# Kernel tuning notes

Hardware: AMD Instinct MI355X
Metric: run time of the kernel (lower is better)

The kernel has to match this reference:

```python
import jax, jax.numpy as jnp
import numpy as np
import math

B, S, E = 2, 2048, 2048
H = 16
DH = E // H            # 128
L = 64                 # latent_dim
EB = 128               # effective block size (== block_size, adjuster init = log(block_size))
KB = 4 * EB            # kv block size = 512


def setup_inputs() -> dict:
    key = jax.random.key(0)
    ks = jax.random.split(key, 16)
    s_e = 1.0 / math.sqrt(E)
    s_dh = 1.0 / math.sqrt(DH)
    return {
        "x": jax.random.normal(ks[0], (B, S, E), jnp.float32),
        "Wq": jax.random.normal(ks[1], (E, E), jnp.float32) * s_e,
        "bq": jnp.zeros((E,), jnp.float32),
        "Wk": jax.random.normal(ks[2], (E, E), jnp.float32) * s_e,
        "bk": jnp.zeros((E,), jnp.float32),
        "Wv": jax.random.normal(ks[3], (E, E), jnp.float32) * s_e,
        "bv": jnp.zeros((E,), jnp.float32),
        "Wo": jax.random.normal(ks[4], (E, E), jnp.float32) * s_e,
        "bo": jnp.zeros((E,), jnp.float32),
        "Wql": jax.random.normal(ks[5], (DH, L), jnp.float32) * s_dh,
        "bql": jnp.zeros((L,), jnp.float32),
        "Wkl": jax.random.normal(ks[6], (DH, L), jnp.float32) * s_dh,
        "bkl": jnp.zeros((L,), jnp.float32),
        "Wm": jax.random.normal(ks[7], (DH, DH), jnp.float32) * s_dh,
        "bm": jnp.zeros((DH,), jnp.float32),
    }


def _split_heads(t):
    # [B,S,E] -> [B,H,S,DH]
    return t.reshape(B, S, H, DH).transpose(0, 2, 1, 3)


def reference(x, Wq, bq, Wk, bk, Wv, bv, Wo, bo, Wql, bql, Wkl, bkl, Wm, bm):
    q = _split_heads(x @ Wq + bq)
    k = _split_heads(x @ Wk + bk)
    v = _split_heads(x @ Wv + bv)

    # elu+1 feature maps on latent projections
    q_lat = jax.nn.elu(q @ Wql + bql) + 1.0  # [B,H,S,L]
    k_lat = jax.nn.elu(k @ Wkl + bkl) + 1.0  # [B,H,S,L]

    nq, nk = S // EB, S // KB
    qb = q_lat.reshape(B, H, nq, EB, L)
    kb = k_lat.reshape(B, H, nk, KB, L)
    vb = v.reshape(B, H, nk, KB, DH)

    scale = 1.0 / math.sqrt(L)
    # per-(q block, kv block) scores: [B,H,nq,nk,EB,KB]
    scores = jnp.einsum("bhqel,bhkfl->bhqkef", qb, kb) * scale
    # softmax independently over each kv block (axis = f), then SUM over kv blocks
    probs = jax.nn.softmax(scores, axis=-1)
    out = jnp.einsum("bhqkef,bhkfd->bhqed", probs, vb)  # [B,H,nq,EB,DH]
    out = out.reshape(B, H, S, DH)

    # latent mixer: Linear(head_dim) -> gelu
    mixed = jax.nn.gelu(out @ Wm + bm)

    y = mixed.transpose(0, 2, 1, 3).reshape(B, S, E)
    return y @ Wo + bo
```

## Files before the change

### kernel.cpp

```cpp
#include <hip/hip_runtime.h>
#include <stdint.h>
#include <math.h>

#define B_ 2
#define S_ 2048
#define E_ 2048
#define H_ 16
#define DH_ 128
#define L_ 64

typedef unsigned short u16;
typedef __attribute__((ext_vector_type(4))) float f32x4;
typedef __attribute__((ext_vector_type(8))) short short8;
typedef __attribute__((ext_vector_type(4))) short short4v;

__device__ __forceinline__ u16 f2bf(float f) {
    union { float f; uint32_t u; } c; c.f = f;
    uint32_t u = c.u + 0x7fff + ((c.u >> 16) & 1);
    return (u16)(u >> 16);
}
__device__ __forceinline__ u16 f2bf_ru(float f) {
    union { float f; uint32_t u; } c; c.f = f;
    return (u16)((c.u + 0x8000u) >> 16);
}
__device__ __forceinline__ float bf2f(u16 h) {
    union { uint32_t u; float f; } c; c.u = ((uint32_t)h) << 16;
    return c.f;
}
__device__ __forceinline__ float elu1(float x) {
    return x > 0.f ? x + 1.f : __expf(x);
}
__device__ __forceinline__ float gelu_tanh(float x) {
    float z = 0.7978845608028654f * (x + 0.044715f * x * x * x);
    float az = fabsf(z);
    float e = __expf(-2.f * az);
    float t = (1.f - e) / (1.f + e);
    t = (z >= 0.f) ? t : -t;
    return 0.5f * x * (1.f + t);
}
__device__ __forceinline__ void async16(u16* lds_dst, const u16* g_src) {
    __builtin_amdgcn_global_load_lds(
        (const __attribute__((address_space(1))) uint32_t*)g_src,
        (__attribute__((address_space(3))) uint32_t*)lds_dst, 16, 0, 0);
}
__device__ __forceinline__ int swz_off(int row, int chunk) {
    return ((chunk ^ (row & 7)) << 3);
}

__global__ __launch_bounds__(256) void cvt_bf16(const float* __restrict__ in,
                                                u16* __restrict__ out, int n8) {
    for (int i = blockIdx.x * 256 + threadIdx.x; i < n8; i += gridDim.x * 256) {
        float4 a = reinterpret_cast<const float4*>(in)[2 * i];
        float4 b = reinterpret_cast<const float4*>(in)[2 * i + 1];
        u16 u[8] __attribute__((aligned(16)));
        u[0] = f2bf(a.x); u[1] = f2bf(a.y); u[2] = f2bf(a.z); u[3] = f2bf(a.w);
        u[4] = f2bf(b.x); u[5] = f2bf(b.y); u[6] = f2bf(b.z); u[7] = f2bf(b.w);
        reinterpret_cast<int4*>(out)[i] = *(const int4*)u;
    }
}

__device__ void wtrans_body(u16* sp, const float* __restrict__ W,
                            u16* __restrict__ Wt, int K, int N, int bx, int by) {
    const int tid = threadIdx.x;
    const int n0 = bx * 64, k0 = by * 64;
    const int c4 = (tid & 15) * 4, r = tid >> 4;
    #pragma unroll
    for (int i = 0; i < 4; i++) {
        int row = r + 16 * i;
        float4 v = *reinterpret_cast<const float4*>(&W[(size_t)(k0 + row) * N + n0 + c4]);
        sp[(c4 + 0) * 68 + row] = f2bf(v.x); sp[(c4 + 1) * 68 + row] = f2bf(v.y);
        sp[(c4 + 2) * 68 + row] = f2bf(v.z); sp[(c4 + 3) * 68 + row] = f2bf(v.w);
    }
    __syncthreads();
    #pragma unroll
    for (int i = 0; i < 4; i++) {
        int nr = r + 16 * i;
        ushort4 o = *reinterpret_cast<const ushort4*>(&sp[nr * 68 + c4]);
        *reinterpret_cast<ushort4*>(&Wt[(size_t)(n0 + nr) * K + k0 + c4]) = o;
    }
}

__global__ __launch_bounds__(256) void wtrans(const float* __restrict__ W,
                                              u16* __restrict__ Wt, int K, int N) {
    __shared__ u16 sp[64 * 68];
    wtrans_body(sp, W, Wt, K, N, blockIdx.x, blockIdx.y);
}

__global__ __launch_bounds__(256) void small_prep(
    const float* __restrict__ Wm, const float* __restrict__ Wql,
    const float* __restrict__ Wkl, const float* __restrict__ bq,
    const float* __restrict__ bk, const float* __restrict__ bv,
    const float* __restrict__ bql, const float* __restrict__ bkl,
    u16* __restrict__ Wmt, u16* __restrict__ Wqlt, u16* __restrict__ Wklt,
    float* __restrict__ beff)
{
    __shared__ u16 sp[64 * 68];
    const int blk = blockIdx.x, tid = threadIdx.x;
    if (blk < 4) {
        wtrans_body(sp, Wm, Wmt, 128, 128, blk & 1, blk >> 1);
    } else if (blk < 6) {
        wtrans_body(sp, Wql, Wqlt, 128, 64, 0, blk - 4);
    } else if (blk < 8) {
        wtrans_body(sp, Wkl, Wklt, 128, 64, 0, blk - 6);
    } else if (blk < 16) {
        const float* b  = (blk < 12) ? bq : bk;
        const float* Wl = (blk < 12) ? Wql : Wkl;
        const float* bl = (blk < 12) ? bql : bkl;
        int outoff = (blk < 12) ? 0 : 1024;
        int t = ((blk - 8) & 3) * 256 + tid;
        int h = t >> 6, n = t & 63;
        float s = bl[n];
        for (int d = 0; d < 128; d++) s += b[h * 128 + d] * Wl[d * 64 + n];
        beff[outoff + t] = s;
    } else {
        int t = (blk - 16) * 256 + tid;
        int h = t >> 7, n = t & 127;
        float s = 0.f;
        for (int d = 0; d < 128; d++) s += bv[h * 128 + d] * Wm[d * 128 + n];
        beff[2048 + t] = s;
    }
}

__device__ void weff_body(u16* lds, const float* __restrict__ W,
                          const u16* __restrict__ Wlt, u16* __restrict__ Wefft,
                          int outoff, int kblk, int h)
{
    const int tid = threadIdx.x, l = tid & 63, w = tid >> 6;
    const int k0 = kblk * 128;

    #pragma unroll
    for (int i = 0; i < 4; i++) {
        int lin = i * 256 + tid, row = lin >> 4, c = lin & 15;
        async16(&lds[lin * 8], &Wlt[row * 128 + swz_off(row, c)]);
    }
    #pragma unroll
    for (int i = 0; i < 16; i++) {
        int e = (i * 256 + tid) * 4;
        int row = e >> 7, ec = e & 127;
        float4 v4 = *reinterpret_cast<const float4*>(
            &W[(size_t)(k0 + row) * E_ + h * DH_ + ec]);
        u16 u[4] __attribute__((aligned(8)));
        u[0] = f2bf(v4.x); u[1] = f2bf(v4.y); u[2] = f2bf(v4.z); u[3] = f2bf(v4.w);
        int chunk = ec >> 3, half = (ec >> 2) & 1;
        *reinterpret_cast<uint64_t*>(
            &lds[8192 + row * 128 + swz_off(row, chunk) + half * 4]) = *(const uint64_t*)u;
    }
    __syncthreads();

    f32x4 zero = {0.f, 0.f, 0.f, 0.f};
    f32x4 acc[8];
    #pragma unroll
    for (int nt = 0; nt < 8; nt++) acc[nt] = zero;
    #pragma unroll
    for (int ks = 0; ks < 4; ks++) {
        int arow = 16 * w + (l & 15);
        short8 af = *reinterpret_cast<const short8*>(
            &lds[arow * 128 + swz_off(arow, ks * 4 + (l >> 4))]);
        #pragma unroll
        for (int nt = 0; nt < 8; nt++) {
            int brow = 16 * nt + (l & 15);
            short8 bf = *reinterpret_cast<const short8*>(
                &lds[8192 + brow * 128 + swz_off(brow, ks * 4 + (l >> 4))]);
            acc[nt] = __builtin_amdgcn_mfma_f32_16x16x32_bf16(af, bf, acc[nt], 0, 0, 0);
        }
    }
    #pragma unroll
    for (int nt = 0; nt < 8; nt++) {
        int kc = k0 + 16 * nt + (l & 15);
        #pragma unroll
        for (int j = 0; j < 4; j++) {
            int nl = 16 * w + (l >> 4) * 4 + j;
            Wefft[(size_t)(outoff + h * 64 + nl) * E_ + kc] = f2bf(acc[nt][j]);
        }
    }
}

__device__ void weffv_body(u16* lds, const float* __restrict__ Wv,
                           const u16* __restrict__ Wmt, u16* __restrict__ Wv2t,
                           int eblk, int h)
{
    const int tid = threadIdx.x, l = tid & 63, w = tid >> 6;
    const int e0 = eblk * 128;

    #pragma unroll
    for (int i = 0; i < 8; i++) {
        int lin = i * 256 + tid, row = lin >> 4, c = lin & 15;
        async16(&lds[lin * 8], &Wmt[row * 128 + swz_off(row, c)]);
    }
    #pragma unroll
    for (int i = 0; i < 16; i++) {
        int e = (i * 256 + tid) * 4;
        int row = e >> 7, ec = e & 127;
        float4 v4 = *reinterpret_cast<const float4*>(
            &Wv[(size_t)(e0 + row) * E_ + h * DH_ + ec]);
        u16 u[4] __attribute__((aligned(8)));
        u[0] = f2bf(v4.x); u[1] = f2bf(v4.y); u[2] = f2bf(v4.z); u[3] = f2bf(v4.w);
        int chunk = ec >> 3, half = (ec >> 2) & 1;
        *reinterpret_cast<uint64_t*>(
            &lds[16384 + row * 128 + swz_off(row, chunk) + half * 4]) = *(const uint64_t*)u;
    }
    __syncthreads();

    f32x4 zero = {0.f, 0.f, 0.f, 0.f};
    f32x4 acc[2][8];
    #pragma unroll
    for (int mi = 0; mi < 2; mi++)
        #pragma unroll
        for (int nt = 0; nt < 8; nt++) acc[mi][nt] = zero;
    #pragma unroll
    for (int ks = 0; ks < 4; ks++) {
        short8 af[2];
        #pragma unroll
        for (int mi = 0; mi < 2; mi++) {
            int arow = 32 * w + 16 * mi + (l & 15);
            af[mi] = *reinterpret_cast<const short8*>(
                &lds[arow * 128 + swz_off(arow, ks * 4 + (l >> 4))]);
        }
        #pragma unroll
        for (int nt = 0; nt < 8; nt++) {
            int brow = 16 * nt + (l & 15);
            short8 bf = *reinterpret_cast<const short8*>(
                &lds[16384 + brow * 128 + swz_off(brow, ks * 4 + (l >> 4))]);
            #pragma unroll
            for (int mi = 0; mi < 2; mi++)
                acc[mi][nt] = __builtin_amdgcn_mfma_f32_16x16x32_bf16(af[mi], bf, acc[mi][nt], 0, 0, 0);
        }
    }
    #pragma unroll
    for (int mi = 0; mi < 2; mi++)
        #pragma unroll
        for (int nt = 0; nt < 8; nt++) {
            int ec = e0 + 16 * nt + (l & 15);
            #pragma unroll
            for (int j = 0; j < 4; j++) {
                int dp = 32 * w + 16 * mi + (l >> 4) * 4 + j;
                Wv2t[(size_t)(h * 128 + dp) * E_ + ec] = f2bf(acc[mi][nt][j]);
            }
        }
}

__global__ __launch_bounds__(256) void weff3(
    const float* __restrict__ Wq, const float* __restrict__ Wk,
    const float* __restrict__ Wv, const u16* __restrict__ Wqlt,
    const u16* __restrict__ Wklt, const u16* __restrict__ Wmt,
    u16* __restrict__ Wefft)
{
    __shared__ u16 lds[32768];
    const int blk = blockIdx.x;
    if (blk < 256) {
        weff_body(lds, Wq, Wqlt, Wefft, 0, blk & 15, blk >> 4);
    } else if (blk < 512) {
        weff_body(lds, Wk, Wklt, Wefft, 1024, (blk - 256) & 15, (blk - 256) >> 4);
    } else {
        weffv_body(lds, Wv, Wmt, Wefft + (size_t)2048 * E_, (blk - 512) & 15, (blk - 512) >> 4);
    }
}

template <typename OutT, int EPI>
__global__ __launch_bounds__(256) void gemm_bf16(
    const u16* __restrict__ A, const u16* __restrict__ Wt,
    const float* __restrict__ bias, OutT* __restrict__ C,
    u16* __restrict__ latq, u16* __restrict__ latk, u16* __restrict__ latv,
    int M, int N, int K)
{
    __shared__ u16 lds[16384];
    const int tid = threadIdx.x, l = tid & 63, w = tid >> 6;
    const int wr = w >> 1, wc = w & 1;
    const int row0 = blockIdx.y * 128, col0 = blockIdx.x * 128;

    f32x4 zero = {0.f, 0.f, 0.f, 0.f};
    f32x4 acc[4][4];
    #pragma unroll
    for (int i = 0; i < 4; i++)
        #pragma unroll
        for (int j = 0; j < 4; j++) acc[i][j] = zero;

    for (int k0 = 0; k0 < K; k0 += 64) {
        #pragma unroll
        for (int i = 0; i < 4; i++) {
            int lin = i * 256 + tid, row = lin >> 3, c = lin & 7;
            int sc = swz_off(row, c);
            async16(&lds[lin * 8], &A[(size_t)(row0 + row) * K + k0 + sc]);
            async16(&lds[8192 + lin * 8], &Wt[(size_t)(col0 + row) * K + k0 + sc]);
        }
        __syncthreads();
        #pragma unroll
        for (int ks = 0; ks < 2; ks++) {
            short8 af[4], bf[4];
            #pragma unroll
            for (int mi = 0; mi < 4; mi++) {
                int row = 64 * wr + 16 * mi + (l & 15);
                af[mi] = *reinterpret_cast<const short8*>(
                    &lds[row * 64 + swz_off(row, ks * 4 + (l >> 4))]);
            }
            #pragma unroll
            for (int ni = 0; ni < 4; ni++) {
                int row = 64 * wc + 16 * ni + (l & 15);
                bf[ni] = *reinterpret_cast<const short8*>(
                    &lds[8192 + row * 64 + swz_off(row, ks * 4 + (l >> 4))]);
            }
            #pragma unroll
            for (int mi = 0; mi < 4; mi++)
                #pragma unroll
                for (int ni = 0; ni < 4; ni++)
                    acc[mi][ni] = __builtin_amdgcn_mfma_f32_16x16x32_bf16(
                        af[mi], bf[ni], acc[mi][ni], 0, 0, 0);
        }
        __syncthreads();
    }
    #pragma unroll
    for (int mi = 0; mi < 4; mi++)
        #pragma unroll
        for (int ni = 0; ni < 4; ni++) {
            int col = col0 + 64 * wc + 16 * ni + (l & 15);
            float bv = bias[col];
            #pragma unroll
            for (int j = 0; j < 4; j++) {
                int row = row0 + 64 * wr + 16 * mi + (l >> 4) * 4 + j;
                float v = acc[mi][ni][j] + bv;
                if (EPI == 1) {
                    int bb = row >> 11, s = row & 2047;
                    if (col < 2048) {
                        v = elu1(v);
                        if (col < 1024) v *= 0.125f;
                        u16* dst = (col < 1024) ? latq : latk;
                        int h = (col >> 6) & 15, n = col & 63;
                        dst[(((size_t)bb * 16 + h) * S_ + s) * 64 + n] = f2bf(v);
                    } else {
                        int c2 = col - 2048;
                        int d = c2 & 127, hh = c2 >> 7;
                        latv[((size_t)((bb << 4) + hh) * 128 + d) * (size_t)S_ + s] = f2bf(v);
                    }
                } else if (sizeof(OutT) == 2) {
                    C[(size_t)row * N + col] = (OutT)f2bf(v);
                } else {
                    C[(size_t)row * N + col] = (OutT)v;
                }
            }
        }
}

__global__ __launch_bounds__(256, 2) void attn_mfma(
    const u16* __restrict__ qlat, const u16* __restrict__ klat,
    const u16* __restrict__ Vt, const float* __restrict__ bm,
    u16* __restrict__ mixed)
{
    __shared__ u16 pool[32768];
    const int tid = threadIdx.x, l = tid & 63, w = tid >> 6;
    const int g = l >> 4;
    const int qi = blockIdx.x, bh = blockIdx.y;
    const int bb = bh >> 4, h = bh & 15;
    const u16* klat_bh = klat + (size_t)bh * S_ * L_;
    const u16* vt_bh = Vt + (size_t)bh * 128 * S_;
    const int q0 = qi * 128;

    #pragma unroll
    for (int i = 0; i < 4; i++) {
        int lin = i * 256 + tid, row = lin >> 3, c = lin & 7;
        async16(&pool[lin * 8],
                &qlat[((size_t)bh * S_ + q0 + row) * 64 + swz_off(row, c)]);
    }
    #pragma unroll
    for (int i = 0; i < 2; i++) {
        int lin = i * 256 + tid, row = lin >> 3, c = lin & 7;
        async16(&pool[8192 + lin * 8], &klat_bh[(size_t)row * 64 + swz_off(row, c)]);
    }
    #pragma unroll
    for (int i = 0; i < 4; i++) {
        int lin = i * 256 + tid, d = lin >> 3, c = lin & 7;
        async16(&pool[16384 + lin * 8], &vt_bh[(size_t)d * S_ + swz_off(d, c)]);
    }
    __syncthreads();

    short8 qf[2][2];
    #pragma unroll
    for (int qt = 0; qt < 2; qt++)
        #pragma unroll
        for (int ks = 0; ks < 2; ks++) {
            int row = 32 * w + 16 * qt + (l & 15);
            qf[qt][ks] = *reinterpret_cast<const short8*>(
                &pool[row * 64 + swz_off(row, ks * 4 + g)]);
        }

    f32x4 zero = {0.f, 0.f, 0.f, 0.f};
    f32x4 Ot[8][2], Op[8][2];
    float l_reg[2];
    #pragma unroll
    for (int nd = 0; nd < 8; nd++)
        #pragma unroll
        for (int qt = 0; qt < 2; qt++) { Ot[nd][qt] = zero; Op[nd][qt] = zero; }
    #pragma unroll
    for (int qt = 0; qt < 2; qt++) l_reg[qt] = 0.f;

    for (int t = 0; t < 32; t++) {
        const int cur = t & 1;
        if (t < 31) {
            const int f0 = (t + 1) * 64, nb = cur ^ 1;
            #pragma unroll
            for (int i = 0; i < 2; i++) {
                int lin = i * 256 + tid, row = lin >> 3, c = lin & 7;
                async16(&pool[8192 + nb * 4096 + lin * 8],
                        &klat_bh[(size_t)(f0 + row) * 64 + swz_off(row, c)]);
            }
            #pragma unroll
            for (int i = 0; i < 4; i++) {
                int lin = i * 256 + tid, d = lin >> 3, c = lin & 7;
                async16(&pool[16384 + nb * 8192 + lin * 8],
                        &vt_bh[(size_t)d * S_ + f0 + swz_off(d, c)]);
            }
        }
        const u16* Kb = &pool[8192 + cur * 4096];
        const u16* Vb = &pool[16384 + cur * 8192];

        f32x4 accS[4][2];
        #pragma unroll
        for (int fi = 0; fi < 4; fi++)
            #pragma unroll
            for (int qt = 0; qt < 2; qt++) accS[fi][qt] = zero;
        #pragma unroll
        for (int ks = 0; ks < 2; ks++) {
            short8 kfrag[4];
            #pragma unroll
            for (int fi = 0; fi < 4; fi++) {
                int row = 16 * fi + (l & 15);
                kfrag[fi] = *reinterpret_cast<const short8*>(
                    &Kb[row * 64 + swz_off(row, ks * 4 + g)]);
            }
            #pragma unroll
            for (int fi = 0; fi < 4; fi++)
                #pragma unroll
                for (int qt = 0; qt < 2; qt++)
                    accS[fi][qt] = __builtin_amdgcn_mfma_f32_16x16x32_bf16(
                        kfrag[fi], qf[qt][ks], accS[fi][qt], 0, 0, 0);
        }

        short4v pf[2][4];
        #pragma unroll
        for (int qt = 0; qt < 2; qt++) {
            float sum = 0.f;
            #pragma unroll
            for (int fi = 0; fi < 4; fi++) {
                float p[4];
                #pragma unroll
                for (int j = 0; j < 4; j++) {
                    p[j] = __expf(accS[fi][qt][j]);
                    sum += p[j];
                }
                short4v pk;
                pk[0] = (short)f2bf_ru(p[0]); pk[1] = (short)f2bf_ru(p[1]);
                pk[2] = (short)f2bf_ru(p[2]); pk[3] = (short)f2bf_ru(p[3]);
                pf[qt][fi] = pk;
            }
            sum += __shfl_xor(sum, 16);
            sum += __shfl_xor(sum, 32);
            l_reg[qt] += sum;
        }

        #pragma unroll
        for (int kt = 0; kt < 4; kt++) {
            int fl = 16 * kt + 4 * g;
            int fch = fl >> 3, fsub = fl & 7;
            #pragma unroll
            for (int nd = 0; nd < 8; nd++) {
                int d = 16 * nd + (l & 15);
                short4v vfrag = *reinterpret_cast<const short4v*>(
                    &Vb[d * 64 + ((fch ^ (d & 7)) << 3) + fsub]);
                #pragma unroll
                for (int qt = 0; qt < 2; qt++)
                    Op[nd][qt] = __builtin_amdgcn_mfma_f32_16x16x16bf16_1k(
                        vfrag, pf[qt][kt], Op[nd][qt], 0, 0, 0);
            }
        }

        if ((t & 7) == 7) {
            #pragma unroll
            for (int qt = 0; qt < 2; qt++) {
                float linv = 1.f / l_reg[qt];
                #pragma unroll
                for (int nd = 0; nd < 8; nd++) {
                    Ot[nd][qt] += Op[nd][qt] * linv;
                    Op[nd][qt] = zero;
                }
                l_reg[qt] = 0.f;
            }
        }
        __syncthreads();
    }

    #pragma unroll
    for (int nd = 0; nd < 8; nd++)
        #pragma unroll
        for (int qt = 0; qt < 2; qt++) {
            int q = q0 + 32 * w + 16 * qt + (l & 15);
            u16 hi4[4] __attribute__((aligned(8)));
            #pragma unroll
            for (int j = 0; j < 4; j++) {
                int d = 16 * nd + 4 * g + j;
                float v = gelu_tanh(Ot[nd][qt][j] + bm[d]);
                hi4[j] = f2bf(v);
            }
            size_t o = ((size_t)(bb * S_ + q)) * E_ + h * DH_ + 16 * nd + 4 * g;
            *reinterpret_cast<ushort4*>(&mixed[o]) = *(const ushort4*)hi4;
        }
}

extern "C" void kernel_launch(void* const* d_in, const int* in_sizes, int n_in,
                              void* d_out, int out_size, void* d_ws, size_t ws_size,
                              hipStream_t stream)
{
    const float* x   = (const float*)d_in[0];
    const float* Wq  = (const float*)d_in[1];
    const float* bq  = (const float*)d_in[2];
    const float* Wk  = (const float*)d_in[3];
    const float* bk  = (const float*)d_in[4];
    const float* Wv  = (const float*)d_in[5];
    const float* bv  = (const float*)d_in[6];
    const float* Wo  = (const float*)d_in[7];
    const float* bo  = (const float*)d_in[8];
    const float* Wql = (const float*)d_in[9];
    const float* bql = (const float*)d_in[10];
    const float* Wkl = (const float*)d_in[11];
    const float* bkl = (const float*)d_in[12];
    const float* Wm  = (const float*)d_in[13];
    const float* bm  = (const float*)d_in[14];
    float* out = (float*)d_out;

    u16* ws0   = (u16*)d_ws;
    u16* xb    = ws0;
    u16* Wefft = ws0 + 8388608;
    u16* Wot   = Wefft + 8388608;
    u16* Wmt   = Wot + 4194304;
    u16* Wqlt  = Wmt + 16384;
    u16* Wklt  = Wqlt + 8192;
    float* beff = (float*)(Wklt + 8192);
    u16* Vt    = (u16*)(beff + 4096);
    u16* qlat  = Vt + 8388608;
    u16* klat  = qlat + 4194304;
    u16* mixed = xb;

    dim3 proj_g(32, 32);
    dim3 gemm_g(16, 32);
    dim3 attn_g(16, 32);

    cvt_bf16<<<2048, 256, 0, stream>>>(x, xb, 1048576);
    wtrans<<<dim3(32, 32), 256, 0, stream>>>(Wo, Wot, 2048, 2048);
    small_prep<<<24, 256, 0, stream>>>(Wm, Wql, Wkl, bq, bk, bv, bql, bkl,
                                       Wmt, Wqlt, Wklt, beff);
    weff3<<<768, 256, 0, stream>>>(Wq, Wk, Wv, Wqlt, Wklt, Wmt, Wefft);

    gemm_bf16<u16, 1><<<proj_g, 256, 0, stream>>>(
        xb, Wefft, beff, (u16*)nullptr, qlat, klat, Vt, 4096, 4096, 2048);
    attn_mfma<<<attn_g, 256, 0, stream>>>(qlat, klat, Vt, bm, mixed);
    gemm_bf16<float, 0><<<gemm_g, 256, 0, stream>>>(
        mixed, Wot, bo, out, nullptr, nullptr, nullptr, 4096, 2048, 2048);
}
```

Measured before the change: 277.9 us.

## Merge prep kernels and compute V projection transposed for coalesced Vt stores

Three preprocessing kernels (x to bf16 conversion, Wo transpose, small weight prep) are folded into one launch with block-range dispatch, which cuts launch overhead. The projection GEMM is split into a latent Q/K part and a V part. The V part computes Weff_v·x^T, so each output row lands along the sequence dimension of Vt and the transposed Vt write becomes contiguous instead of strided. Blocks of the two parts are interleaved by parity. This adds divergent epilogue paths and per-row bias loads in the V branch.

New measurement: 251.6 us. -9.5%, faster.

```diff
diff --git a/kernel.cpp b/kernel.cpp
--- a/kernel.cpp
+++ b/kernel.cpp
@@ -47,18 +47,6 @@
     return ((chunk ^ (row & 7)) << 3);
 }
 
-__global__ __launch_bounds__(256) void cvt_bf16(const float* __restrict__ in,
-                                                u16* __restrict__ out, int n8) {
-    for (int i = blockIdx.x * 256 + threadIdx.x; i < n8; i += gridDim.x * 256) {
-        float4 a = reinterpret_cast<const float4*>(in)[2 * i];
-        float4 b = reinterpret_cast<const float4*>(in)[2 * i + 1];
-        u16 u[8] __attribute__((aligned(16)));
-        u[0] = f2bf(a.x); u[1] = f2bf(a.y); u[2] = f2bf(a.z); u[3] = f2bf(a.w);
-        u[4] = f2bf(b.x); u[5] = f2bf(b.y); u[6] = f2bf(b.z); u[7] = f2bf(b.w);
-        reinterpret_cast<int4*>(out)[i] = *(const int4*)u;
-    }
-}
-
 __device__ void wtrans_body(u16* sp, const float* __restrict__ W,
                             u16* __restrict__ Wt, int K, int N, int bx, int by) {
     const int tid = threadIdx.x;
@@ -80,13 +68,9 @@
     }
 }
 
-__global__ __launch_bounds__(256) void wtrans(const float* __restrict__ W,
-                                              u16* __restrict__ Wt, int K, int N) {
-    __shared__ u16 sp[64 * 68];
-    wtrans_body(sp, W, Wt, K, N, blockIdx.x, blockIdx.y);
-}
-
-__global__ __launch_bounds__(256) void small_prep(
+__global__ __launch_bounds__(256) void prep1(
+    const float* __restrict__ x, u16* __restrict__ xb,
+    const float* __restrict__ Wo, u16* __restrict__ Wot,
     const float* __restrict__ Wm, const float* __restrict__ Wql,
     const float* __restrict__ Wkl, const float* __restrict__ bq,
     const float* __restrict__ bk, const float* __restrict__ bv,
@@ -96,28 +80,43 @@
 {
     __shared__ u16 sp[64 * 68];
     const int blk = blockIdx.x, tid = threadIdx.x;
-    if (blk < 4) {
-        wtrans_body(sp, Wm, Wmt, 128, 128, blk & 1, blk >> 1);
-    } else if (blk < 6) {
-        wtrans_body(sp, Wql, Wqlt, 128, 64, 0, blk - 4);
-    } else if (blk < 8) {
-        wtrans_body(sp, Wkl, Wklt, 128, 64, 0, blk - 6);
-    } else if (blk < 16) {
-        const float* b  = (blk < 12) ? bq : bk;
-        const float* Wl = (blk < 12) ? Wql : Wkl;
-        const float* bl = (blk < 12) ? bql : bkl;
-        int outoff = (blk < 12) ? 0 : 1024;
-        int t = ((blk - 8) & 3) * 256 + tid;
-        int h = t >> 6, n = t & 63;
-        float s = bl[n];
-        for (int d = 0; d < 128; d++) s += b[h * 128 + d] * Wl[d * 64 + n];
-        beff[outoff + t] = s;
+    if (blk < 2048) {
+        for (int i = blk * 256 + tid; i < 1048576; i += 2048 * 256) {
+            float4 a = reinterpret_cast<const float4*>(x)[2 * i];
+            float4 b = reinterpret_cast<const float4*>(x)[2 * i + 1];
+            u16 u[8] __attribute__((aligned(16)));
+            u[0] = f2bf(a.x); u[1] = f2bf(a.y); u[2] = f2bf(a.z); u[3] = f2bf(a.w);
+            u[4] = f2bf(b.x); u[5] = f2bf(b.y); u[6] = f2bf(b.z); u[7] = f2bf(b.w);
+            reinterpret_cast<int4*>(xb)[i] = *(const int4*)u;
+        }
+    } else if (blk < 3072) {
+        int t = blk - 2048;
+        wtrans_body(sp, Wo, Wot, 2048, 2048, t & 31, t >> 5);
     } else {
-        int t = (blk - 16) * 256 + tid;
-        int h = t >> 7, n = t & 127;
-        float s = 0.f;
-        for (int d = 0; d < 128; d++) s += bv[h * 128 + d] * Wm[d * 128 + n];
-        beff[2048 + t] = s;
+        int b2 = blk - 3072;
+        if (b2 < 4) {
+            wtrans_body(sp, Wm, Wmt, 128, 128, b2 & 1, b2 >> 1);
+        } else if (b2 < 6) {
+            wtrans_body(sp, Wql, Wqlt, 128, 64, 0, b2 - 4);
+        } else if (b2 < 8) {
+            wtrans_body(sp, Wkl, Wklt, 128, 64, 0, b2 - 6);
+        } else if (b2 < 16) {
+            const float* b  = (b2 < 12) ? bq : bk;
+            const float* Wl = (b2 < 12) ? Wql : Wkl;
+            const float* bl = (b2 < 12) ? bql : bkl;
+            int outoff = (b2 < 12) ? 0 : 1024;
+            int t = ((b2 - 8) & 3) * 256 + tid;
+            int h = t >> 6, n = t & 63;
+            float s = bl[n];
+            for (int d = 0; d < 128; d++) s += b[h * 128 + d] * Wl[d * 64 + n];
+            beff[outoff + t] = s;
+        } else {
+            int t = (b2 - 16) * 256 + tid;
+            int h = t >> 7, n = t & 127;
+            float s = 0.f;
+            for (int d = 0; d < 128; d++) s += bv[h * 128 + d] * Wm[d * 128 + n];
+            beff[2048 + t] = s;
+        }
     }
 }
 
@@ -256,11 +255,99 @@
     }
 }
 
-template <typename OutT, int EPI>
-__global__ __launch_bounds__(256) void gemm_bf16(
+__global__ __launch_bounds__(256) void proj2(
+    const u16* __restrict__ xb, const u16* __restrict__ Wefft,
+    const float* __restrict__ beff,
+    u16* __restrict__ latq, u16* __restrict__ latk, u16* __restrict__ Vt)
+{
+    __shared__ u16 lds[16384];
+    const int tid = threadIdx.x, l = tid & 63, w = tid >> 6;
+    const int wr = w >> 1, wc = w & 1;
+    const int blk = blockIdx.x;
+    const bool isV = blk & 1;
+    const int sub = blk >> 1;
+    const u16* A;
+    const u16* Wt;
+    const float* bias;
+    int row0, col0;
+    if (!isV) {
+        A = xb; Wt = Wefft; bias = beff;
+        col0 = (sub & 15) * 128; row0 = (sub >> 4) * 128;
+    } else {
+        A = Wefft + (size_t)2048 * E_; Wt = xb; bias = beff + 2048;
+        col0 = (sub & 31) * 128; row0 = (sub >> 5) * 128;
+    }
+
+    f32x4 zero = {0.f, 0.f, 0.f, 0.f};
+    f32x4 acc[4][4];
+    #pragma unroll
+    for (int i = 0; i < 4; i++)
+        #pragma unroll
+        for (int j = 0; j < 4; j++) acc[i][j] = zero;
+
+    for (int k0 = 0; k0 < 2048; k0 += 64) {
+        #pragma unroll
+        for (int i = 0; i < 4; i++) {
+            int lin = i * 256 + tid, row = lin >> 3, c = lin & 7;
+            int sc = swz_off(row, c);
+            async16(&lds[lin * 8], &A[(size_t)(row0 + row) * 2048 + k0 + sc]);
+            async16(&lds[8192 + lin * 8], &Wt[(size_t)(col0 + row) * 2048 + k0 + sc]);
+        }
+        __syncthreads();
+        #pragma unroll
+        for (int ks = 0; ks < 2; ks++) {
+            short8 af[4], bf[4];
+            #pragma unroll
+            for (int mi = 0; mi < 4; mi++) {
+                int row = 64 * wr + 16 * mi + (l & 15);
+                af[mi] = *reinterpret_cast<const short8*>(
+                    &lds[row * 64 + swz_off(row, ks * 4 + (l >> 4))]);
+            }
+            #pragma unroll
+            for (int ni = 0; ni < 4; ni++) {
+                int row = 64 * wc + 16 * ni + (l & 15);
+                bf[ni] = *reinterpret_cast<const short8*>(
+                    &lds[8192 + row * 64 + swz_off(row, ks * 4 + (l >> 4))]);
+            }
+            #pragma unroll
+            for (int mi = 0; mi < 4; mi++)
+                #pragma unroll
+                for (int ni = 0; ni < 4; ni++)
+                    acc[mi][ni] = __builtin_amdgcn_mfma_f32_16x16x32_bf16(
+                        af[mi], bf[ni], acc[mi][ni], 0, 0, 0);
+        }
+        __syncthreads();
+    }
+
+    #pragma unroll
+    for (int mi = 0; mi < 4; mi++)
+        #pragma unroll
+        for (int ni = 0; ni < 4; ni++) {
+            int col = col0 + 64 * wc + 16 * ni + (l & 15);
+            float bv = isV ? 0.f : bias[col];
+            #pragma unroll
+            for (int j = 0; j < 4; j++) {
+                int row = row0 + 64 * wr + 16 * mi + (l >> 4) * 4 + j;
+                float v = acc[mi][ni][j] + (isV ? bias[row] : bv);
+                if (!isV) {
+                    v = elu1(v);
+                    if (col < 1024) v *= 0.125f;
+                    u16* dst = (col < 1024) ? latq : latk;
+                    int h = (col >> 6) & 15, n = col & 63;
+                    int bb = row >> 11, s = row & 2047;
+                    dst[(((size_t)bb * 16 + h) * S_ + s) * 64 + n] = f2bf(v);
+                } else {
+                    int d = row & 127, hh = row >> 7;
+                    int bb = col >> 11, s = col & 2047;
+                    Vt[((size_t)((bb << 4) + hh) * 128 + d) * (size_t)S_ + s] = f2bf(v);
+                }
+            }
+        }
+}
+
+__global__ __launch_bounds__(256) void gemm_final(
     const u16* __restrict__ A, const u16* __restrict__ Wt,
-    const float* __restrict__ bias, OutT* __restrict__ C,
-    u16* __restrict__ latq, u16* __restrict__ latk, u16* __restrict__ latv,
+    const float* __restrict__ bias, float* __restrict__ C,
     int M, int N, int K)
 {
     __shared__ u16 lds[16384];
@@ -317,25 +404,7 @@
             #pragma unroll
             for (int j = 0; j < 4; j++) {
                 int row = row0 + 64 * wr + 16 * mi + (l >> 4) * 4 + j;
-                float v = acc[mi][ni][j] + bv;
-                if (EPI == 1) {
-                    int bb = row >> 11, s = row & 2047;
-                    if (col < 2048) {
-                        v = elu1(v);
-                        if (col < 1024) v *= 0.125f;
-                        u16* dst = (col < 1024) ? latq : latk;
-                        int h = (col >> 6) & 15, n = col & 63;
-                        dst[(((size_t)bb * 16 + h) * S_ + s) * 64 + n] = f2bf(v);
-                    } else {
-                        int c2 = col - 2048;
-                        int d = c2 & 127, hh = c2 >> 7;
-                        latv[((size_t)((bb << 4) + hh) * 128 + d) * (size_t)S_ + s] = f2bf(v);
-                    }
-                } else if (sizeof(OutT) == 2) {
-                    C[(size_t)row * N + col] = (OutT)f2bf(v);
-                } else {
-                    C[(size_t)row * N + col] = (OutT)v;
-                }
+                C[(size_t)row * N + col] = acc[mi][ni][j] + bv;
             }
         }
 }
@@ -538,19 +607,14 @@
     u16* klat  = qlat + 4194304;
     u16* mixed = xb;
 
-    dim3 proj_g(32, 32);
     dim3 gemm_g(16, 32);
     dim3 attn_g(16, 32);
 
-    cvt_bf16<<<2048, 256, 0, stream>>>(x, xb, 1048576);
-    wtrans<<<dim3(32, 32), 256, 0, stream>>>(Wo, Wot, 2048, 2048);
-    small_prep<<<24, 256, 0, stream>>>(Wm, Wql, Wkl, bq, bk, bv, bql, bkl,
-                                       Wmt, Wqlt, Wklt, beff);
+    prep1<<<3096, 256, 0, stream>>>(x, xb, Wo, Wot, Wm, Wql, Wkl,
+                                    bq, bk, bv, bql, bkl,
+                                    Wmt, Wqlt, Wklt, beff);
     weff3<<<768, 256, 0, stream>>>(Wq, Wk, Wv, Wqlt, Wklt, Wmt, Wefft);
-
-    gemm_bf16<u16, 1><<<proj_g, 256, 0, stream>>>(
-        xb, Wefft, beff, (u16*)nullptr, qlat, klat, Vt, 4096, 4096, 2048);
+    proj2<<<1024, 256, 0, stream>>>(xb, Wefft, beff, qlat, klat, Vt);
     attn_mfma<<<attn_g, 256, 0, stream>>>(qlat, klat, Vt, bm, mixed);
-    gemm_bf16<float, 0><<<gemm_g, 256, 0, stream>>>(
-        mixed, Wot, bo, out, nullptr, nullptr, nullptr, 4096, 2048, 2048);
-}
+    gemm_final<<<gemm_g, 256, 0, stream>>>(mixed, Wot, bo, out, 4096, 2048, 2048);
+}
```
